# Performance work log

Hardware: AMD Instinct MI355X
Metric: run time of the kernel (lower is better)

Reference implementation:

```python
import jax, jax.numpy as jnp
import numpy as np

DIM = 1536
NH = 12
HD = DIM // NH  # 128
B = 1
F, H, W = 8, 16, 16
S = F * H * W  # 2048
EPS = 1e-6
MAX_POS = 1024


def _rmsnorm(x, g):
    # WanRMSNorm: x * rsqrt(mean(x^2, -1) + eps) * weight  (computed in fp32)
    return x * jax.lax.rsqrt(jnp.mean(x * x, axis=-1, keepdims=True) + EPS) * g


def _rope_apply(x, grid_sizes, freqs):
    # x: [B, S, NH, HD]; freqs: [1024, HD//2] angles. Full (level-0) freqs_i path.
    f, h, w = [int(v) for v in np.asarray(grid_sizes[0])]
    c = HD // 2  # 64
    s0 = c - 2 * (c // 3)  # 22 (frame freqs)
    s1 = c // 3            # 21 (height / width freqs)
    p0 = freqs[:f, :s0]
    p1 = freqs[:h, s0:s0 + s1]
    p2 = freqs[:w, s0 + s1:]
    ang = jnp.concatenate([
        jnp.broadcast_to(p0[:, None, None, :], (f, h, w, s0)),
        jnp.broadcast_to(p1[None, :, None, :], (f, h, w, s1)),
        jnp.broadcast_to(p2[None, None, :, :], (f, h, w, s1)),
    ], axis=-1).reshape(f * h * w, 1, c)  # [S, 1, c]
    cos, sin = jnp.cos(ang), jnp.sin(ang)
    xr = x[0].reshape(S, NH, c, 2)  # pairs -> complex rotation
    x0, x1 = xr[..., 0], xr[..., 1]
    out = jnp.stack([x0 * cos - x1 * sin, x0 * sin + x1 * cos], axis=-1)
    return out.reshape(S, NH, HD)[None].astype(jnp.float32)  # [1, S, NH, HD]


def setup_inputs() -> dict:
    key = jax.random.key(0)
    ks = jax.random.split(key, 8)
    sc = 0.02
    return {
        "x": jax.random.normal(ks[0], (B, S, DIM), jnp.float32),
        "freqs": jax.random.uniform(ks[1], (MAX_POS, HD // 2), jnp.float32, 0.0, 2.0 * np.pi),
        "wq": jax.random.normal(ks[2], (DIM, DIM), jnp.float32) * sc,
        "bq": jnp.zeros((DIM,), jnp.float32),
        "wk": jax.random.normal(ks[3], (DIM, DIM), jnp.float32) * sc,
        "bk": jnp.zeros((DIM,), jnp.float32),
        "wv": jax.random.normal(ks[4], (DIM, DIM), jnp.float32) * sc,
        "bv": jnp.zeros((DIM,), jnp.float32),
        "wo": jax.random.normal(ks[5], (DIM, DIM), jnp.float32) * sc,
        "bo": jnp.zeros((DIM,), jnp.float32),
        "gq": jnp.ones((DIM,), jnp.float32),
        "gk": jnp.ones((DIM,), jnp.float32),
        "seq_lens": jnp.array([S], jnp.int32),
        "grid_sizes": jnp.array([[F, H, W]], jnp.int32),
    }


def reference(x, freqs, wq, bq, wk, bk, wv, bv, wo, bo, gq, gk, seq_lens, grid_sizes):
    b, s = x.shape[:2]
    q = _rmsnorm(x @ wq.T + bq, gq).reshape(b, s, NH, HD)
    k = _rmsnorm(x @ wk.T + bk, gk).reshape(b, s, NH, HD)
    v = (x @ wv.T + bv).reshape(b, s, NH, HD)
    q = _rope_apply(q, grid_sizes, freqs)
    k = _rope_apply(k, grid_sizes, freqs)
    # flash_attention with k_lens=seq_lens, full window -> masked SDPA
    kmask = jnp.arange(s)[None, :] < seq_lens[:, None]  # [b, s]
    scores = jnp.einsum('bqnd,bknd->bnqk', q, k) / np.sqrt(HD).astype(np.float32)
    scores = jnp.where(kmask[:, None, None, :], scores, jnp.finfo(scores.dtype).min)
    attn = jax.nn.softmax(scores, axis=-1)
    out = jnp.einsum('bnqk,bknd->bqnd', attn, v).reshape(b, s, DIM)
    return out @ wo.T + bo
```

## Files before the change

kernel.cpp:

```cpp
#include <hip/hip_runtime.h>
#include <math.h>

#define DIMN 1536
#define NHEAD 12
#define HDIM 128
#define SLEN 2048
#define EPSV 1e-6f

typedef __attribute__((ext_vector_type(8))) short short8;
typedef __attribute__((ext_vector_type(4))) short short4v;
typedef __attribute__((ext_vector_type(4))) float f32x4;

typedef __attribute__((address_space(1))) const void gvoid_t;
typedef __attribute__((address_space(3))) void lvoid_t;

__device__ __forceinline__ void gload_lds16(const void* g, void* l) {
    __builtin_amdgcn_global_load_lds((gvoid_t*)g, (lvoid_t*)l, 16, 0, 0);
}

__device__ inline short to_bf16(float f) {
    union { float f; unsigned u; } v; v.f = f;
    unsigned r = (v.u + 0x7FFFu + ((v.u >> 16) & 1u)) >> 16;
    return (short)r;
}
__device__ inline float bf_to_f(short h) {
    union { unsigned u; float f; } v;
    v.u = ((unsigned)(unsigned short)h) << 16;
    return v.f;
}

__device__ __forceinline__ int swz8(int row, int c) {
    return c ^ (row & 7);
}

__global__ __launch_bounds__(256)
void cast5(const float* s0, const float* s1, const float* s2,
           const float* s3, const float* s4,
           short* d0, short* d1, short* d2, short* d3, short* d4,
           int n0, int nw)
{
    const float* s; short* d; int n;
    switch (blockIdx.y) {
        case 0: s = s0; d = d0; n = n0; break;
        case 1: s = s1; d = d1; n = nw; break;
        case 2: s = s2; d = d2; n = nw; break;
        case 3: s = s3; d = d3; n = nw; break;
        default: s = s4; d = d4; n = nw; break;
    }
    int idx = (blockIdx.x * 256 + threadIdx.x) * 8;
    if (idx >= n) return;
    float4 a = *(const float4*)(s + idx);
    float4 b = *(const float4*)(s + idx + 4);
    short8 r;
    r[0] = to_bf16(a.x); r[1] = to_bf16(a.y); r[2] = to_bf16(a.z); r[3] = to_bf16(a.w);
    r[4] = to_bf16(b.x); r[5] = to_bf16(b.y); r[6] = to_bf16(b.z); r[7] = to_bf16(b.w);
    *(short8*)(d + idx) = r;
}

__device__ __forceinline__ void gemm_mainloop(const short* __restrict__ A,
    const short* __restrict__ W, int m0, int n0, int K,
    short* As, short* Bs, f32x4 (&acc)[4][4])
{
    const int tid = threadIdx.x;
    const int wave = tid >> 6, lane = tid & 63;
    const int quad = lane >> 4, col = lane & 15;
    const int wm = wave >> 1, wn = wave & 1;
    const int sr = tid >> 3;
    const int sc = tid & 7;

    for (int kt = 0; kt < K; kt += 64) {
        __syncthreads();
        #pragma unroll
        for (int i = 0; i < 4; ++i) {
            const int row = i * 32 + sr;
            const int c = swz8(row, sc);
            gload_lds16(A + (size_t)(m0 + row) * K + kt + c * 8, As + i * 2048 + tid * 8);
        }
        #pragma unroll
        for (int i = 0; i < 4; ++i) {
            const int row = i * 32 + sr;
            const int c = swz8(row, sc);
            gload_lds16(W + (size_t)(n0 + row) * K + kt + c * 8, Bs + i * 2048 + tid * 8);
        }
        __syncthreads();

        #pragma unroll
        for (int kb = 0; kb < 2; ++kb) {
            short8 af[4], bf[4];
            #pragma unroll
            for (int mt = 0; mt < 4; ++mt) {
                const int row = wm * 64 + mt * 16 + col;
                af[mt] = *(const short8*)&As[row * 64 + swz8(row, kb * 4 + quad) * 8];
            }
            #pragma unroll
            for (int nt = 0; nt < 4; ++nt) {
                const int row = wn * 64 + nt * 16 + col;
                bf[nt] = *(const short8*)&Bs[row * 64 + swz8(row, kb * 4 + quad) * 8];
            }
            #pragma unroll
            for (int mt = 0; mt < 4; ++mt)
                #pragma unroll
                for (int nt = 0; nt < 4; ++nt)
                    acc[mt][nt] = __builtin_amdgcn_mfma_f32_16x16x32_bf16(
                        af[mt], bf[nt], acc[mt][nt], 0, 0, 0);
        }
    }
}

__global__ __launch_bounds__(256)
void gemm_qkv(const short* __restrict__ A,
              const short* __restrict__ W0, const short* __restrict__ W1,
              const short* __restrict__ W2,
              const float* __restrict__ b0, const float* __restrict__ b1,
              const float* __restrict__ b2,
              short* __restrict__ Y0, short* __restrict__ Y1,
              short* __restrict__ Vp)
{
    __shared__ __attribute__((aligned(16))) short As[128 * 64];
    __shared__ __attribute__((aligned(16))) short Bs[128 * 64];

    const int sel = blockIdx.x / (DIMN / 128);
    const int nb  = blockIdx.x % (DIMN / 128);
    const short* W    = (sel == 0) ? W0 : (sel == 1) ? W1 : W2;
    const float* bias = (sel == 0) ? b0 : (sel == 1) ? b1 : b2;

    const int tid = threadIdx.x;
    const int wave = tid >> 6, lane = tid & 63;
    const int quad = lane >> 4, col = lane & 15;
    const int wm = wave >> 1, wn = wave & 1;
    const int m0 = blockIdx.y * 128, n0 = nb * 128;

    f32x4 acc[4][4];
    #pragma unroll
    for (int i = 0; i < 4; ++i)
        #pragma unroll
        for (int j = 0; j < 4; ++j)
            #pragma unroll
            for (int r = 0; r < 4; ++r) acc[i][j][r] = 0.f;

    gemm_mainloop(A, W, m0, n0, DIMN, As, Bs, acc);

    if (sel < 2) {
        short* Y = (sel == 0) ? Y0 : Y1;
        #pragma unroll
        for (int mt = 0; mt < 4; ++mt) {
            #pragma unroll
            for (int nt = 0; nt < 4; ++nt) {
                const int n = n0 + wn * 64 + nt * 16 + col;
                const float bb = bias[n];
                #pragma unroll
                for (int r = 0; r < 4; ++r) {
                    const int m = m0 + wm * 64 + mt * 16 + quad * 4 + r;
                    Y[(size_t)m * DIMN + n] = to_bf16(acc[mt][nt][r] + bb);
                }
            }
        }
    } else {
        const int head = nb;
        const int kt64 = blockIdx.y * 2 + wm;
        #pragma unroll
        for (int mt = 0; mt < 4; ++mt) {
            #pragma unroll
            for (int nt = 0; nt < 4; ++nt) {
                const int n = n0 + wn * 64 + nt * 16 + col;
                const float bb = bias[n];
                const int dt = wn * 4 + nt;
                const int chunk = (head * 32 + kt64) * 16 + dt * 2 + (mt >> 1);
                const int off = ((mt & 1) * 2 + (quad >> 1)) * 128 + col * 8 + (quad & 1) * 4;
                short4v o;
                #pragma unroll
                for (int r = 0; r < 4; ++r) o[r] = to_bf16(acc[mt][nt][r] + bb);
                *(short4v*)(Vp + (size_t)chunk * 512 + off) = o;
            }
        }
    }
}

__global__ __launch_bounds__(256)
void gemm_out(const short* __restrict__ A, const short* __restrict__ W,
              const float* __restrict__ bias, float* __restrict__ Yf)
{
    __shared__ __attribute__((aligned(16))) short As[128 * 64];
    __shared__ __attribute__((aligned(16))) short Bs[128 * 64];

    const int tid = threadIdx.x;
    const int wave = tid >> 6, lane = tid & 63;
    const int quad = lane >> 4, col = lane & 15;
    const int wm = wave >> 1, wn = wave & 1;
    const int m0 = blockIdx.y * 128, n0 = blockIdx.x * 128;

    f32x4 acc[4][4];
    #pragma unroll
    for (int i = 0; i < 4; ++i)
        #pragma unroll
        for (int j = 0; j < 4; ++j)
            #pragma unroll
            for (int r = 0; r < 4; ++r) acc[i][j][r] = 0.f;

    gemm_mainloop(A, W, m0, n0, DIMN, As, Bs, acc);

    #pragma unroll
    for (int mt = 0; mt < 4; ++mt) {
        #pragma unroll
        for (int nt = 0; nt < 4; ++nt) {
            const int n = n0 + wn * 64 + nt * 16 + col;
            const float bb = bias[n];
            #pragma unroll
            for (int r = 0; r < 4; ++r) {
                const int m = m0 + wm * 64 + mt * 16 + quad * 4 + r;
                Yf[(size_t)m * DIMN + n] = acc[mt][nt][r] + bb;
            }
        }
    }
}

__global__ __launch_bounds__(256)
void rms_rope_qk(short* __restrict__ qbuf, const short* __restrict__ kbuf,
                 short* __restrict__ Kp,
                 const float* __restrict__ gq, const float* __restrict__ gk,
                 const float* __restrict__ freqs, const int* __restrict__ grid_sizes)
{
    const int s = blockIdx.x;
    const int isK = blockIdx.y;
    const int tid = threadIdx.x;
    short* qrow = qbuf + (size_t)s * DIMN;
    const short* row = isK ? (kbuf + (size_t)s * DIMN) : qrow;
    const float* g = isK ? gk : gq;

    float ss = 0.f;
    if (tid < 192) {
        short8 v = *(const short8*)(row + tid * 8);
        #pragma unroll
        for (int j = 0; j < 8; ++j) { float f = bf_to_f(v[j]); ss += f * f; }
    }
    #pragma unroll
    for (int off = 32; off; off >>= 1) ss += __shfl_down(ss, off, 64);

    __shared__ float red[4];
    __shared__ float s_scale;
    if ((tid & 63) == 0) red[tid >> 6] = ss;
    __syncthreads();
    if (tid == 0) {
        float t = red[0] + red[1] + red[2] + red[3];
        float sc = rsqrtf(t / (float)DIMN + EPSV);
        s_scale = isK ? sc : sc * 0.08838834764831845f;
    }
    __syncthreads();
    const float scale = s_scale;

    const int h = grid_sizes[1], w = grid_sizes[2];
    const int fi = s / (h * w);
    const int hi = (s / w) % h;
    const int wi = s % w;

    if (!isK) {
        for (int p = tid; p < NHEAD * 64; p += 256) {
            const int n = p >> 6;
            const int d = p & 63;
            const int idx = (d < 22) ? fi : ((d < 43) ? hi : wi);
            const float ang = freqs[idx * 64 + d];
            float sn, cs;
            __sincosf(ang, &sn, &cs);
            const int base = n * HDIM + 2 * d;
            const float v0 = bf_to_f(qrow[base]) * scale * g[base];
            const float v1 = bf_to_f(qrow[base + 1]) * scale * g[base + 1];
            qrow[base]     = to_bf16(v0 * cs - v1 * sn);
            qrow[base + 1] = to_bf16(v0 * sn + v1 * cs);
        }
    } else if (tid < 192) {
        const int n = tid >> 4;
        const int o = tid & 15;
        short8 outv;
        #pragma unroll
        for (int pp = 0; pp < 4; ++pp) {
            const int pd = o * 4 + pp;
            const int idx = (pd < 22) ? fi : ((pd < 43) ? hi : wi);
            const float ang = freqs[idx * 64 + pd];
            float sn, cs;
            __sincosf(ang, &sn, &cs);
            const int base = n * HDIM + 2 * pd;
            const float v0 = bf_to_f(row[base]) * scale * g[base];
            const float v1 = bf_to_f(row[base + 1]) * scale * g[base + 1];
            outv[pp * 2]     = to_bf16(v0 * cs - v1 * sn);
            outv[pp * 2 + 1] = to_bf16(v0 * sn + v1 * cs);
        }
        const int kb = s >> 4, colk = s & 15;
        const int kc = o >> 2, quadk = o & 3;
        const size_t addr = ((((size_t)(n * 128 + kb) * 4 + kc) * 64) + quadk * 16 + colk) * 8;
        *(short8*)(Kp + addr) = outv;
    }
}

__global__ __launch_bounds__(128)
void attn_mfma6(const short* __restrict__ Q, const short* __restrict__ Kp,
                const short* __restrict__ Vp, short* __restrict__ O,
                const int* __restrict__ seq_lens)
{
    __shared__ __attribute__((aligned(16))) char smem[32768 + 2 * 16 * 72 * 2];
    short* KL = (short*)smem;
    short* VL = (short*)(smem + 16384);
    short* Ps = (short*)(smem + 32768);

    const int tid = threadIdx.x;
    const int wave = tid >> 6, lane = tid & 63;
    const int quad = lane >> 4, col = lane & 15;
    const int head = blockIdx.y;
    const int row0 = blockIdx.x * 32 + wave * 16;
    const int slen = seq_lens[0];
    short* psw = Ps + wave * (16 * 72);

    short8 qf[4];
    #pragma unroll
    for (int kc = 0; kc < 4; ++kc)
        qf[kc] = *(const short8*)(Q + (size_t)(row0 + col) * DIMN
                                  + head * HDIM + kc * 32 + quad * 8);

    f32x4 oacc[8];
    #pragma unroll
    for (int dt = 0; dt < 8; ++dt)
        #pragma unroll
        for (int r = 0; r < 4; ++r) oacc[dt][r] = 0.f;
    float lsum[4] = {0.f, 0.f, 0.f, 0.f};

    for (int kt64 = 0; kt64 < SLEN / 64; ++kt64) {
        __syncthreads();
        {
            const char* ks = (const char*)Kp + ((size_t)(head * 128 + kt64 * 4) * 4) * 1024;
            const char* vs = (const char*)Vp + ((size_t)(head * 32 + kt64) * 16) * 1024;
            #pragma unroll
            for (int i = 0; i < 8; ++i)
                gload_lds16(ks + i * 2048 + tid * 16, smem + i * 2048 + tid * 16);
            #pragma unroll
            for (int i = 0; i < 8; ++i)
                gload_lds16(vs + i * 2048 + tid * 16, smem + 16384 + i * 2048 + tid * 16);
        }
        __syncthreads();

        f32x4 s[4];
        #pragma unroll
        for (int nt = 0; nt < 4; ++nt)
            #pragma unroll
            for (int r = 0; r < 4; ++r) s[nt][r] = 0.f;

        #pragma unroll
        for (int kc = 0; kc < 4; ++kc) {
            short8 kf[4];
            #pragma unroll
            for (int nt = 0; nt < 4; ++nt)
                kf[nt] = *(const short8*)&KL[(nt * 4 + kc) * 512 + lane * 8];
            #pragma unroll
            for (int nt = 0; nt < 4; ++nt)
                s[nt] = __builtin_amdgcn_mfma_f32_16x16x32_bf16(qf[kc], kf[nt], s[nt], 0, 0, 0);
        }

        const int kt = kt64 * 64;
        #pragma unroll
        for (int nt = 0; nt < 4; ++nt) {
            const bool masked = (kt + nt * 16 + col >= slen);
            #pragma unroll
            for (int r = 0; r < 4; ++r) {
                float p = masked ? 0.f : __expf(s[nt][r]);
                lsum[r] += p;
                psw[(quad * 4 + r) * 72 + nt * 16 + col] = to_bf16(p);
            }
        }

        short8 pf[2];
        #pragma unroll
        for (int kc = 0; kc < 2; ++kc)
            pf[kc] = *(const short8*)&psw[col * 72 + kc * 32 + quad * 8];

        #pragma unroll
        for (int dt = 0; dt < 8; ++dt) {
            short8 vf[2];
            #pragma unroll
            for (int kc = 0; kc < 2; ++kc)
                vf[kc] = *(const short8*)&VL[(dt * 2 + kc) * 512 + lane * 8];
            #pragma unroll
            for (int kc = 0; kc < 2; ++kc)
                oacc[dt] = __builtin_amdgcn_mfma_f32_16x16x32_bf16(pf[kc], vf[kc], oacc[dt], 0, 0, 0);
        }
    }

    float inv[4];
    #pragma unroll
    for (int r = 0; r < 4; ++r) {
        #pragma unroll
        for (int off = 8; off; off >>= 1) lsum[r] += __shfl_xor(lsum[r], off, 64);
        inv[r] = 1.0f / lsum[r];
    }
    #pragma unroll
    for (int dt = 0; dt < 8; ++dt) {
        #pragma unroll
        for (int r = 0; r < 4; ++r) {
            O[(size_t)(row0 + quad * 4 + r) * DIMN + head * HDIM + dt * 16 + col]
                = to_bf16(oacc[dt][r] * inv[r]);
        }
    }
}

extern "C" void kernel_launch(void* const* d_in, const int* in_sizes, int n_in,
                              void* d_out, int out_size, void* d_ws, size_t ws_size,
                              hipStream_t stream)
{
    const float* x     = (const float*)d_in[0];
    const float* freqs = (const float*)d_in[1];
    const float* wq    = (const float*)d_in[2];
    const float* bq    = (const float*)d_in[3];
    const float* wk    = (const float*)d_in[4];
    const float* bk    = (const float*)d_in[5];
    const float* wv    = (const float*)d_in[6];
    const float* bv    = (const float*)d_in[7];
    const float* wo    = (const float*)d_in[8];
    const float* bo    = (const float*)d_in[9];
    const float* gq    = (const float*)d_in[10];
    const float* gk    = (const float*)d_in[11];
    const int* seq_lens   = (const int*)d_in[12];
    const int* grid_sizes = (const int*)d_in[13];
    float* out = (float*)d_out;

    const size_t NX = (size_t)SLEN * DIMN;
    const size_t NW = (size_t)DIMN * DIMN;
    short* xb  = (short*)d_ws;
    short* wqb = xb + NX;
    short* wkb = wqb + NW;
    short* wvb = wkb + NW;
    short* wob = wvb + NW;
    short* qb  = wob + NW;
    short* kb  = qb + NX;
    short* vp  = kb + NX;
    short* kp  = vp + NX;
    short* ob  = kp + NX;

    cast5<<<dim3(1536, 5), 256, 0, stream>>>(x, wq, wk, wv, wo,
                                             xb, wqb, wkb, wvb, wob,
                                             (int)NX, (int)NW);

    gemm_qkv<<<dim3(3 * DIMN / 128, SLEN / 128), 256, 0, stream>>>(
        xb, wqb, wkb, wvb, bq, bk, bv, qb, kb, vp);

    rms_rope_qk<<<dim3(SLEN, 2), 256, 0, stream>>>(qb, kb, kp, gq, gk, freqs, grid_sizes);

    attn_mfma6<<<dim3(SLEN / 32, NHEAD), 128, 0, stream>>>(qb, kp, vp, ob, seq_lens);

    gemm_out<<<dim3(DIMN / 128, SLEN / 128), 256, 0, stream>>>(ob, wob, bo, out);
}
```

Measured before the change: 273.8 us.

## Triple-buffer K/V tiles in attention with async LDS prefetch two steps ahead

The attention kernel now processes 32-key steps instead of 64 and keeps three LDS buffers, issuing direct global-to-LDS loads for K and V two steps ahead. It waits on vmcnt counters instead of fully synchronising after each load. The V packing layout written by the QKV GEMM changes to match the 32-key chunks. The goal is to hide global load latency behind MFMA work, at the cost of more LDS per block (about 50KB), which may reduce occupancy, and twice as many barriers.

```diff
diff --git a/kernel.cpp b/kernel.cpp
--- a/kernel.cpp
+++ b/kernel.cpp
@@ -165,7 +165,7 @@
                 const int n = n0 + wn * 64 + nt * 16 + col;
                 const float bb = bias[n];
                 const int dt = wn * 4 + nt;
-                const int chunk = (head * 32 + kt64) * 16 + dt * 2 + (mt >> 1);
+                const int chunk = (head * 64 + kt64 * 2 + (mt >> 1)) * 8 + dt;
                 const int off = ((mt & 1) * 2 + (quad >> 1)) * 128 + col * 8 + (quad & 1) * 4;
                 short4v o;
                 #pragma unroll
@@ -292,14 +292,12 @@
 }
 
 __global__ __launch_bounds__(128)
-void attn_mfma6(const short* __restrict__ Q, const short* __restrict__ Kp,
+void attn_mfma7(const short* __restrict__ Q, const short* __restrict__ Kp,
                 const short* __restrict__ Vp, short* __restrict__ O,
                 const int* __restrict__ seq_lens)
 {
-    __shared__ __attribute__((aligned(16))) char smem[32768 + 2 * 16 * 72 * 2];
-    short* KL = (short*)smem;
-    short* VL = (short*)(smem + 16384);
-    short* Ps = (short*)(smem + 32768);
+    __shared__ __attribute__((aligned(16))) char smem[3 * 16384 + 2048];
+    short* Ps = (short*)(smem + 3 * 16384);
 
     const int tid = threadIdx.x;
     const int wave = tid >> 6, lane = tid & 63;
@@ -307,7 +305,7 @@
     const int head = blockIdx.y;
     const int row0 = blockIdx.x * 32 + wave * 16;
     const int slen = seq_lens[0];
-    short* psw = Ps + wave * (16 * 72);
+    short* psw = Ps + wave * (16 * 32);
 
     short8 qf[4];
     #pragma unroll
@@ -322,64 +320,81 @@
         for (int r = 0; r < 4; ++r) oacc[dt][r] = 0.f;
     float lsum[4] = {0.f, 0.f, 0.f, 0.f};
 
-    for (int kt64 = 0; kt64 < SLEN / 64; ++kt64) {
-        __syncthreads();
-        {
-            const char* ks = (const char*)Kp + ((size_t)(head * 128 + kt64 * 4) * 4) * 1024;
-            const char* vs = (const char*)Vp + ((size_t)(head * 32 + kt64) * 16) * 1024;
-            #pragma unroll
-            for (int i = 0; i < 8; ++i)
-                gload_lds16(ks + i * 2048 + tid * 16, smem + i * 2048 + tid * 16);
-            #pragma unroll
-            for (int i = 0; i < 8; ++i)
-                gload_lds16(vs + i * 2048 + tid * 16, smem + 16384 + i * 2048 + tid * 16);
-        }
-        __syncthreads();
-
-        f32x4 s[4];
-        #pragma unroll
-        for (int nt = 0; nt < 4; ++nt)
+    asm volatile("s_waitcnt vmcnt(0)" ::: "memory");
+
+    const char* kbase = (const char*)Kp + ((size_t)head * 128) * 4096;
+    const char* vbase = (const char*)Vp + ((size_t)head * 64) * 8192;
+
+    auto stage = [&](int buf, int step) {
+        const char* ks = kbase + (size_t)step * 8192;
+        const char* vs = vbase + (size_t)step * 8192;
+        char* dk = smem + buf * 16384;
+        #pragma unroll
+        for (int i = 0; i < 4; ++i)
+            gload_lds16(ks + i * 2048 + tid * 16, dk + i * 2048 + tid * 16);
+        #pragma unroll
+        for (int i = 0; i < 4; ++i)
+            gload_lds16(vs + i * 2048 + tid * 16, dk + 8192 + i * 2048 + tid * 16);
+    };
+
+    const int NSTEP = SLEN / 32;
+    stage(0, 0);
+    stage(1, 1);
+
+    int cur = 0;
+    for (int kt = 0; kt < NSTEP; ++kt) {
+        if (kt + 2 < NSTEP) {
+            int nb = cur + 2; if (nb >= 3) nb -= 3;
+            stage(nb, kt + 2);
+            asm volatile("s_waitcnt vmcnt(16)" ::: "memory");
+        } else if (kt + 1 < NSTEP) {
+            asm volatile("s_waitcnt vmcnt(8)" ::: "memory");
+        } else {
+            asm volatile("s_waitcnt vmcnt(0)" ::: "memory");
+        }
+        __builtin_amdgcn_sched_barrier(0);
+        __builtin_amdgcn_s_barrier();
+        __builtin_amdgcn_sched_barrier(0);
+
+        const short* KL = (const short*)(smem + cur * 16384);
+        const short* VL = KL + 4096;
+
+        f32x4 s[2];
+        #pragma unroll
+        for (int nt = 0; nt < 2; ++nt)
             #pragma unroll
             for (int r = 0; r < 4; ++r) s[nt][r] = 0.f;
 
         #pragma unroll
         for (int kc = 0; kc < 4; ++kc) {
-            short8 kf[4];
-            #pragma unroll
-            for (int nt = 0; nt < 4; ++nt)
-                kf[nt] = *(const short8*)&KL[(nt * 4 + kc) * 512 + lane * 8];
-            #pragma unroll
-            for (int nt = 0; nt < 4; ++nt)
-                s[nt] = __builtin_amdgcn_mfma_f32_16x16x32_bf16(qf[kc], kf[nt], s[nt], 0, 0, 0);
-        }
-
-        const int kt = kt64 * 64;
-        #pragma unroll
-        for (int nt = 0; nt < 4; ++nt) {
-            const bool masked = (kt + nt * 16 + col >= slen);
+            short8 kf0 = *(const short8*)&KL[kc * 512 + lane * 8];
+            short8 kf1 = *(const short8*)&KL[(4 + kc) * 512 + lane * 8];
+            s[0] = __builtin_amdgcn_mfma_f32_16x16x32_bf16(qf[kc], kf0, s[0], 0, 0, 0);
+            s[1] = __builtin_amdgcn_mfma_f32_16x16x32_bf16(qf[kc], kf1, s[1], 0, 0, 0);
+        }
+
+        const int kt0 = kt * 32;
+        #pragma unroll
+        for (int nt = 0; nt < 2; ++nt) {
+            const bool masked = (kt0 + nt * 16 + col >= slen);
             #pragma unroll
             for (int r = 0; r < 4; ++r) {
                 float p = masked ? 0.f : __expf(s[nt][r]);
                 lsum[r] += p;
-                psw[(quad * 4 + r) * 72 + nt * 16 + col] = to_bf16(p);
-            }
-        }
-
-        short8 pf[2];
-        #pragma unroll
-        for (int kc = 0; kc < 2; ++kc)
-            pf[kc] = *(const short8*)&psw[col * 72 + kc * 32 + quad * 8];
+                psw[(quad * 4 + r) * 32 + nt * 16 + col] = to_bf16(p);
+            }
+        }
+
+        short8 pf = *(const short8*)&psw[col * 32 + quad * 8];
 
         #pragma unroll
         for (int dt = 0; dt < 8; ++dt) {
-            short8 vf[2];
-            #pragma unroll
-            for (int kc = 0; kc < 2; ++kc)
-                vf[kc] = *(const short8*)&VL[(dt * 2 + kc) * 512 + lane * 8];
-            #pragma unroll
-            for (int kc = 0; kc < 2; ++kc)
-                oacc[dt] = __builtin_amdgcn_mfma_f32_16x16x32_bf16(pf[kc], vf[kc], oacc[dt], 0, 0, 0);
-        }
+            short8 vf = *(const short8*)&VL[dt * 512 + lane * 8];
+            oacc[dt] = __builtin_amdgcn_mfma_f32_16x16x32_bf16(pf, vf, oacc[dt], 0, 0, 0);
+        }
+
+        __builtin_amdgcn_s_barrier();
+        cur = cur + 1; if (cur >= 3) cur = 0;
     }
 
     float inv[4];
@@ -441,7 +456,7 @@
 
     rms_rope_qk<<<dim3(SLEN, 2), 256, 0, stream>>>(qb, kb, kp, gq, gk, freqs, grid_sizes);
 
-    attn_mfma6<<<dim3(SLEN / 32, NHEAD), 128, 0, stream>>>(qb, kp, vp, ob, seq_lens);
+    attn_mfma7<<<dim3(SLEN / 32, NHEAD), 128, 0, stream>>>(qb, kp, vp, ob, seq_lens);
 
     gemm_out<<<dim3(DIMN / 128, SLEN / 128), 256, 0, stream>>>(ob, wob, bo, out);
 }
```

Result: no change. 276.7 us (+1.1%).

## Rewrite attention as single-wave kernel with register double-buffered K/V loads

Applied to the files above, without the earlier changes.

Replaces the 128-thread attention kernel, which staged K/V tiles through LDS with block barriers, with a 64-thread single-wave kernel. Each wave handles two 16-row query tiles and loads K/V fragments straight from global memory into registers, double-buffered across 32-key steps. The V pre-pack layout in the QKV GEMM changes to match the new per-step fragment order, and blocks are remapped so neighbouring blocks share a head. This removes LDS staging and block syncs, but raises register pressure and relies on L2 for K/V reuse.

```diff
diff --git a/kernel.cpp b/kernel.cpp
--- a/kernel.cpp
+++ b/kernel.cpp
@@ -165,7 +165,7 @@
                 const int n = n0 + wn * 64 + nt * 16 + col;
                 const float bb = bias[n];
                 const int dt = wn * 4 + nt;
-                const int chunk = (head * 32 + kt64) * 16 + dt * 2 + (mt >> 1);
+                const int chunk = (head * 64 + kt64 * 2 + (mt >> 1)) * 8 + dt;
                 const int off = ((mt & 1) * 2 + (quad >> 1)) * 128 + col * 8 + (quad & 1) * 4;
                 short4v o;
                 #pragma unroll
@@ -291,112 +291,125 @@
     }
 }
 
-__global__ __launch_bounds__(128)
-void attn_mfma6(const short* __restrict__ Q, const short* __restrict__ Kp,
+__global__ __launch_bounds__(64, 1)
+void attn_mfma8(const short* __restrict__ Q, const short* __restrict__ Kp,
                 const short* __restrict__ Vp, short* __restrict__ O,
                 const int* __restrict__ seq_lens)
 {
-    __shared__ __attribute__((aligned(16))) char smem[32768 + 2 * 16 * 72 * 2];
-    short* KL = (short*)smem;
-    short* VL = (short*)(smem + 16384);
-    short* Ps = (short*)(smem + 32768);
-
-    const int tid = threadIdx.x;
-    const int wave = tid >> 6, lane = tid & 63;
+    __shared__ __attribute__((aligned(16))) short psw[2 * 16 * 40];
+
+    const int lane = threadIdx.x;
     const int quad = lane >> 4, col = lane & 15;
-    const int head = blockIdx.y;
-    const int row0 = blockIdx.x * 32 + wave * 16;
+
+    const int orig = blockIdx.y * 64 + blockIdx.x;
+    const int work = (orig & 7) * 96 + (orig >> 3);
+    const int head = work >> 6;
+    const int row0 = (work & 63) * 32;
     const int slen = seq_lens[0];
-    short* psw = Ps + wave * (16 * 72);
-
-    short8 qf[4];
-    #pragma unroll
-    for (int kc = 0; kc < 4; ++kc)
-        qf[kc] = *(const short8*)(Q + (size_t)(row0 + col) * DIMN
-                                  + head * HDIM + kc * 32 + quad * 8);
-
-    f32x4 oacc[8];
-    #pragma unroll
-    for (int dt = 0; dt < 8; ++dt)
-        #pragma unroll
-        for (int r = 0; r < 4; ++r) oacc[dt][r] = 0.f;
-    float lsum[4] = {0.f, 0.f, 0.f, 0.f};
-
-    for (int kt64 = 0; kt64 < SLEN / 64; ++kt64) {
-        __syncthreads();
-        {
-            const char* ks = (const char*)Kp + ((size_t)(head * 128 + kt64 * 4) * 4) * 1024;
-            const char* vs = (const char*)Vp + ((size_t)(head * 32 + kt64) * 16) * 1024;
-            #pragma unroll
-            for (int i = 0; i < 8; ++i)
-                gload_lds16(ks + i * 2048 + tid * 16, smem + i * 2048 + tid * 16);
-            #pragma unroll
-            for (int i = 0; i < 8; ++i)
-                gload_lds16(vs + i * 2048 + tid * 16, smem + 16384 + i * 2048 + tid * 16);
-        }
-        __syncthreads();
-
-        f32x4 s[4];
-        #pragma unroll
-        for (int nt = 0; nt < 4; ++nt)
-            #pragma unroll
-            for (int r = 0; r < 4; ++r) s[nt][r] = 0.f;
-
-        #pragma unroll
-        for (int kc = 0; kc < 4; ++kc) {
-            short8 kf[4];
-            #pragma unroll
-            for (int nt = 0; nt < 4; ++nt)
-                kf[nt] = *(const short8*)&KL[(nt * 4 + kc) * 512 + lane * 8];
-            #pragma unroll
-            for (int nt = 0; nt < 4; ++nt)
-                s[nt] = __builtin_amdgcn_mfma_f32_16x16x32_bf16(qf[kc], kf[nt], s[nt], 0, 0, 0);
-        }
-
-        const int kt = kt64 * 64;
-        #pragma unroll
-        for (int nt = 0; nt < 4; ++nt) {
-            const bool masked = (kt + nt * 16 + col >= slen);
-            #pragma unroll
-            for (int r = 0; r < 4; ++r) {
-                float p = masked ? 0.f : __expf(s[nt][r]);
-                lsum[r] += p;
-                psw[(quad * 4 + r) * 72 + nt * 16 + col] = to_bf16(p);
-            }
-        }
-
-        short8 pf[2];
-        #pragma unroll
-        for (int kc = 0; kc < 2; ++kc)
-            pf[kc] = *(const short8*)&psw[col * 72 + kc * 32 + quad * 8];
+
+    short8 qf[2][4];
+    #pragma unroll
+    for (int T = 0; T < 2; ++T)
+        #pragma unroll
+        for (int kc = 0; kc < 4; ++kc)
+            qf[T][kc] = *(const short8*)(Q + (size_t)(row0 + T * 16 + col) * DIMN
+                                         + head * HDIM + kc * 32 + quad * 8);
+
+    f32x4 oacc[2][8];
+    #pragma unroll
+    for (int T = 0; T < 2; ++T)
+        #pragma unroll
+        for (int dt = 0; dt < 8; ++dt)
+            #pragma unroll
+            for (int r = 0; r < 4; ++r) oacc[T][dt][r] = 0.f;
+    float lsum[2][4];
+    #pragma unroll
+    for (int T = 0; T < 2; ++T)
+        #pragma unroll
+        for (int r = 0; r < 4; ++r) lsum[T][r] = 0.f;
+
+    const short* kbase = Kp + (size_t)head * 262144 + lane * 8;
+    const short* vbase = Vp + (size_t)head * 262144 + lane * 8;
+
+    auto loadKV = [&](short8 (&kf)[8], short8 (&vf)[8], int step) {
+        const short* ks = kbase + (size_t)step * 4096;
+        const short* vs = vbase + (size_t)step * 4096;
+        #pragma unroll
+        for (int c = 0; c < 8; ++c) kf[c] = *(const short8*)(ks + c * 512);
+        #pragma unroll
+        for (int c = 0; c < 8; ++c) vf[c] = *(const short8*)(vs + c * 512);
+    };
+
+    auto compute = [&](short8 (&kf)[8], short8 (&vf)[8], int kt) {
+        f32x4 s[2][2];
+        #pragma unroll
+        for (int T = 0; T < 2; ++T)
+            #pragma unroll
+            for (int nt = 0; nt < 2; ++nt)
+                #pragma unroll
+                for (int r = 0; r < 4; ++r) s[T][nt][r] = 0.f;
+
+        #pragma unroll
+        for (int kc = 0; kc < 4; ++kc)
+            #pragma unroll
+            for (int T = 0; T < 2; ++T) {
+                s[T][0] = __builtin_amdgcn_mfma_f32_16x16x32_bf16(qf[T][kc], kf[kc],     s[T][0], 0, 0, 0);
+                s[T][1] = __builtin_amdgcn_mfma_f32_16x16x32_bf16(qf[T][kc], kf[4 + kc], s[T][1], 0, 0, 0);
+            }
+
+        const int kt0 = kt * 32;
+        #pragma unroll
+        for (int T = 0; T < 2; ++T)
+            #pragma unroll
+            for (int nt = 0; nt < 2; ++nt) {
+                const bool masked = (kt0 + nt * 16 + col >= slen);
+                #pragma unroll
+                for (int r = 0; r < 4; ++r) {
+                    float p = masked ? 0.f : __expf(s[T][nt][r]);
+                    lsum[T][r] += p;
+                    psw[T * 640 + (quad * 4 + r) * 40 + nt * 16 + col] = to_bf16(p);
+                }
+            }
+
+        short8 pf0 = *(const short8*)&psw[col * 40 + quad * 8];
+        short8 pf1 = *(const short8*)&psw[640 + col * 40 + quad * 8];
 
         #pragma unroll
         for (int dt = 0; dt < 8; ++dt) {
-            short8 vf[2];
-            #pragma unroll
-            for (int kc = 0; kc < 2; ++kc)
-                vf[kc] = *(const short8*)&VL[(dt * 2 + kc) * 512 + lane * 8];
-            #pragma unroll
-            for (int kc = 0; kc < 2; ++kc)
-                oacc[dt] = __builtin_amdgcn_mfma_f32_16x16x32_bf16(pf[kc], vf[kc], oacc[dt], 0, 0, 0);
-        }
-    }
-
-    float inv[4];
-    #pragma unroll
-    for (int r = 0; r < 4; ++r) {
-        #pragma unroll
-        for (int off = 8; off; off >>= 1) lsum[r] += __shfl_xor(lsum[r], off, 64);
-        inv[r] = 1.0f / lsum[r];
-    }
-    #pragma unroll
-    for (int dt = 0; dt < 8; ++dt) {
+            oacc[0][dt] = __builtin_amdgcn_mfma_f32_16x16x32_bf16(pf0, vf[dt], oacc[0][dt], 0, 0, 0);
+            oacc[1][dt] = __builtin_amdgcn_mfma_f32_16x16x32_bf16(pf1, vf[dt], oacc[1][dt], 0, 0, 0);
+        }
+    };
+
+    short8 kA[8], vA[8], kB[8], vB[8];
+    loadKV(kA, vA, 0);
+
+    #pragma unroll 1
+    for (int kt = 0; kt < SLEN / 32; kt += 2) {
+        loadKV(kB, vB, kt + 1);
+        compute(kA, vA, kt);
+        loadKV(kA, vA, kt + 2);
+        compute(kB, vB, kt + 1);
+    }
+
+    #pragma unroll
+    for (int T = 0; T < 2; ++T)
         #pragma unroll
         for (int r = 0; r < 4; ++r) {
-            O[(size_t)(row0 + quad * 4 + r) * DIMN + head * HDIM + dt * 16 + col]
-                = to_bf16(oacc[dt][r] * inv[r]);
-        }
-    }
+            #pragma unroll
+            for (int off = 8; off; off >>= 1)
+                lsum[T][r] += __shfl_xor(lsum[T][r], off, 64);
+            lsum[T][r] = 1.0f / lsum[T][r];
+        }
+
+    #pragma unroll
+    for (int T = 0; T < 2; ++T)
+        #pragma unroll
+        for (int dt = 0; dt < 8; ++dt)
+            #pragma unroll
+            for (int r = 0; r < 4; ++r)
+                O[(size_t)(row0 + T * 16 + quad * 4 + r) * DIMN
+                  + head * HDIM + dt * 16 + col] = to_bf16(oacc[T][dt][r] * lsum[T][r]);
 }
 
 extern "C" void kernel_launch(void* const* d_in, const int* in_sizes, int n_in,
@@ -441,7 +454,7 @@
 
     rms_rope_qk<<<dim3(SLEN, 2), 256, 0, stream>>>(qb, kb, kp, gq, gk, freqs, grid_sizes);
 
-    attn_mfma6<<<dim3(SLEN / 32, NHEAD), 128, 0, stream>>>(qb, kp, vp, ob, seq_lens);
+    attn_mfma8<<<dim3(64, NHEAD), 64, 0, stream>>>(qb, kp, vp, ob, seq_lens);
 
     gemm_out<<<dim3(DIMN / 128, SLEN / 128), 256, 0, stream>>>(ob, wob, bo, out);
 }
```

New measurement: 277.6 us. Within noise of the previous version (+1.4%).

## Split attention KV range across two waves with direct global fragment loads

Applied to the files above, without the earlier changes.

Restructures attention so each 128-thread block handles 16 query rows, with the two waves each taking half of the key sequence and merging partial outputs and row sums through LDS at the end. K/V fragments are loaded straight from global memory into registers instead of being staged in LDS, which removes the per-tile block barriers. The V packing layout in the QKV GEMM is changed to match 32-key steps, and block indices are remapped so that XCDs share heads. This doubles the block count and total K/V global traffic, relying on L2 hits, and raises register pressure.

```diff
diff --git a/kernel.cpp b/kernel.cpp
--- a/kernel.cpp
+++ b/kernel.cpp
@@ -165,7 +165,7 @@
                 const int n = n0 + wn * 64 + nt * 16 + col;
                 const float bb = bias[n];
                 const int dt = wn * 4 + nt;
-                const int chunk = (head * 32 + kt64) * 16 + dt * 2 + (mt >> 1);
+                const int chunk = (head * 64 + kt64 * 2 + (mt >> 1)) * 8 + dt;
                 const int off = ((mt & 1) * 2 + (quad >> 1)) * 128 + col * 8 + (quad & 1) * 4;
                 short4v o;
                 #pragma unroll
@@ -291,23 +291,25 @@
     }
 }
 
-__global__ __launch_bounds__(128)
-void attn_mfma6(const short* __restrict__ Q, const short* __restrict__ Kp,
+__global__ __launch_bounds__(128, 3)
+void attn_mfma9(const short* __restrict__ Q, const short* __restrict__ Kp,
                 const short* __restrict__ Vp, short* __restrict__ O,
                 const int* __restrict__ seq_lens)
 {
-    __shared__ __attribute__((aligned(16))) char smem[32768 + 2 * 16 * 72 * 2];
-    short* KL = (short*)smem;
-    short* VL = (short*)(smem + 16384);
-    short* Ps = (short*)(smem + 32768);
-
-    const int tid = threadIdx.x;
-    const int wave = tid >> 6, lane = tid & 63;
+    __shared__ __attribute__((aligned(16))) short psw[2 * 16 * 40];
+    __shared__ __attribute__((aligned(16))) float sacc[16 * 132];
+    __shared__ float sl[16];
+
+    const int tid  = threadIdx.x;
+    const int wave = tid >> 6;
+    const int lane = tid & 63;
     const int quad = lane >> 4, col = lane & 15;
-    const int head = blockIdx.y;
-    const int row0 = blockIdx.x * 32 + wave * 16;
+
+    const int orig = blockIdx.y * 128 + blockIdx.x;
+    const int work = (orig & 7) * 192 + (orig >> 3);
+    const int head = work >> 7;
+    const int row0 = (work & 127) * 16;
     const int slen = seq_lens[0];
-    short* psw = Ps + wave * (16 * 72);
 
     short8 qf[4];
     #pragma unroll
@@ -322,80 +324,86 @@
         for (int r = 0; r < 4; ++r) oacc[dt][r] = 0.f;
     float lsum[4] = {0.f, 0.f, 0.f, 0.f};
 
-    for (int kt64 = 0; kt64 < SLEN / 64; ++kt64) {
-        __syncthreads();
-        {
-            const char* ks = (const char*)Kp + ((size_t)(head * 128 + kt64 * 4) * 4) * 1024;
-            const char* vs = (const char*)Vp + ((size_t)(head * 32 + kt64) * 16) * 1024;
-            #pragma unroll
-            for (int i = 0; i < 8; ++i)
-                gload_lds16(ks + i * 2048 + tid * 16, smem + i * 2048 + tid * 16);
-            #pragma unroll
-            for (int i = 0; i < 8; ++i)
-                gload_lds16(vs + i * 2048 + tid * 16, smem + 16384 + i * 2048 + tid * 16);
-        }
-        __syncthreads();
-
-        f32x4 s[4];
-        #pragma unroll
-        for (int nt = 0; nt < 4; ++nt)
+    const short* kbase = Kp + (size_t)head * 262144 + lane * 8;
+    const short* vbase = Vp + (size_t)head * 262144 + lane * 8;
+    short* pswm = psw + wave * 640;
+
+    const int step0 = wave * 32;
+    #pragma unroll 1
+    for (int kt = 0; kt < 32; ++kt) {
+        const int step = step0 + kt;
+        const short* ks = kbase + (size_t)step * 4096;
+        const short* vs = vbase + (size_t)step * 4096;
+
+        short8 kf[8], vf[8];
+        #pragma unroll
+        for (int c = 0; c < 8; ++c) kf[c] = *(const short8*)(ks + c * 512);
+        #pragma unroll
+        for (int c = 0; c < 8; ++c) vf[c] = *(const short8*)(vs + c * 512);
+
+        f32x4 s[2];
+        #pragma unroll
+        for (int nt = 0; nt < 2; ++nt)
             #pragma unroll
             for (int r = 0; r < 4; ++r) s[nt][r] = 0.f;
 
         #pragma unroll
         for (int kc = 0; kc < 4; ++kc) {
-            short8 kf[4];
-            #pragma unroll
-            for (int nt = 0; nt < 4; ++nt)
-                kf[nt] = *(const short8*)&KL[(nt * 4 + kc) * 512 + lane * 8];
-            #pragma unroll
-            for (int nt = 0; nt < 4; ++nt)
-                s[nt] = __builtin_amdgcn_mfma_f32_16x16x32_bf16(qf[kc], kf[nt], s[nt], 0, 0, 0);
-        }
-
-        const int kt = kt64 * 64;
-        #pragma unroll
-        for (int nt = 0; nt < 4; ++nt) {
-            const bool masked = (kt + nt * 16 + col >= slen);
+            s[0] = __builtin_amdgcn_mfma_f32_16x16x32_bf16(qf[kc], kf[kc],     s[0], 0, 0, 0);
+            s[1] = __builtin_amdgcn_mfma_f32_16x16x32_bf16(qf[kc], kf[4 + kc], s[1], 0, 0, 0);
+        }
+
+        const int kt0 = step * 32;
+        #pragma unroll
+        for (int nt = 0; nt < 2; ++nt) {
+            const bool masked = (kt0 + nt * 16 + col >= slen);
             #pragma unroll
             for (int r = 0; r < 4; ++r) {
                 float p = masked ? 0.f : __expf(s[nt][r]);
                 lsum[r] += p;
-                psw[(quad * 4 + r) * 72 + nt * 16 + col] = to_bf16(p);
-            }
-        }
-
-        short8 pf[2];
-        #pragma unroll
-        for (int kc = 0; kc < 2; ++kc)
-            pf[kc] = *(const short8*)&psw[col * 72 + kc * 32 + quad * 8];
-
-        #pragma unroll
-        for (int dt = 0; dt < 8; ++dt) {
-            short8 vf[2];
-            #pragma unroll
-            for (int kc = 0; kc < 2; ++kc)
-                vf[kc] = *(const short8*)&VL[(dt * 2 + kc) * 512 + lane * 8];
-            #pragma unroll
-            for (int kc = 0; kc < 2; ++kc)
-                oacc[dt] = __builtin_amdgcn_mfma_f32_16x16x32_bf16(pf[kc], vf[kc], oacc[dt], 0, 0, 0);
-        }
-    }
-
-    float inv[4];
+                pswm[(quad * 4 + r) * 40 + nt * 16 + col] = to_bf16(p);
+            }
+        }
+
+        short8 pf = *(const short8*)&pswm[col * 40 + quad * 8];
+
+        #pragma unroll
+        for (int dt = 0; dt < 8; ++dt)
+            oacc[dt] = __builtin_amdgcn_mfma_f32_16x16x32_bf16(pf, vf[dt], oacc[dt], 0, 0, 0);
+    }
+
     #pragma unroll
     for (int r = 0; r < 4; ++r) {
         #pragma unroll
-        for (int off = 8; off; off >>= 1) lsum[r] += __shfl_xor(lsum[r], off, 64);
-        inv[r] = 1.0f / lsum[r];
-    }
-    #pragma unroll
-    for (int dt = 0; dt < 8; ++dt) {
-        #pragma unroll
-        for (int r = 0; r < 4; ++r) {
-            O[(size_t)(row0 + quad * 4 + r) * DIMN + head * HDIM + dt * 16 + col]
-                = to_bf16(oacc[dt][r] * inv[r]);
-        }
+        for (int off = 8; off; off >>= 1)
+            lsum[r] += __shfl_xor(lsum[r], off, 64);
+    }
+
+    if (wave == 1) {
+        #pragma unroll
+        for (int dt = 0; dt < 8; ++dt)
+            #pragma unroll
+            for (int r = 0; r < 4; ++r)
+                sacc[(quad * 4 + r) * 132 + dt * 16 + col] = oacc[dt][r];
+        if (col == 0) {
+            #pragma unroll
+            for (int r = 0; r < 4; ++r) sl[quad * 4 + r] = lsum[r];
+        }
+    }
+    __syncthreads();
+    if (wave == 0) {
+        float inv[4];
+        #pragma unroll
+        for (int r = 0; r < 4; ++r)
+            inv[r] = 1.0f / (lsum[r] + sl[quad * 4 + r]);
+        #pragma unroll
+        for (int dt = 0; dt < 8; ++dt)
+            #pragma unroll
+            for (int r = 0; r < 4; ++r) {
+                const float o = oacc[dt][r] + sacc[(quad * 4 + r) * 132 + dt * 16 + col];
+                O[(size_t)(row0 + quad * 4 + r) * DIMN + head * HDIM + dt * 16 + col]
+                    = to_bf16(o * inv[r]);
+            }
     }
 }
 
@@ -441,7 +449,7 @@
 
     rms_rope_qk<<<dim3(SLEN, 2), 256, 0, stream>>>(qb, kb, kp, gq, gk, freqs, grid_sizes);
 
-    attn_mfma6<<<dim3(SLEN / 32, NHEAD), 128, 0, stream>>>(qb, kp, vp, ob, seq_lens);
+    attn_mfma9<<<dim3(128, NHEAD), 128, 0, stream>>>(qb, kp, vp, ob, seq_lens);
 
     gemm_out<<<dim3(DIMN / 128, SLEN / 128), 256, 0, stream>>>(ob, wob, bo, out);
 }
```

Result: no change. 270.5 us (-1.2%).
